# Kernel optimization log

Measured on AMD Instinct MI355X. Metric: run time of the kernel, lower is better.

## Reference

```python
import jax, jax.numpy as jnp
import numpy as np

IN_F, OUT_F = 128, 128
R, LEV, N = 2, 2, 8192
JD = (R - 1) * LEV + 1  # 3 filter levels


def setup_inputs() -> dict:
    key = jax.random.key(0)
    ks = jax.random.split(key, 7)
    x = jax.random.normal(ks[0], (N, IN_F), dtype=jnp.float32)
    d_list = jax.random.uniform(ks[1], (JD, N), dtype=jnp.float32)
    U = jax.random.normal(ks[2], (N, N), dtype=jnp.float32)
    Vt = jax.random.normal(ks[3], (N, N), dtype=jnp.float32)
    # learned params
    bound = float(np.sqrt(6.0 / (IN_F + OUT_F)))  # xavier_uniform
    weight = jax.random.uniform(ks[4], (IN_F, OUT_F), dtype=jnp.float32, minval=-bound, maxval=bound)
    filt = jax.random.uniform(ks[5], (JD, N), dtype=jnp.float32, minval=0.9, maxval=1.1)
    bias = jnp.zeros((OUT_F,), dtype=jnp.float32)
    return {"x": x, "d_list": d_list, "U": U, "Vt": Vt, "weight": weight, "filt": filt, "bias": bias}


def reference(x, d_list, U, Vt, weight, filt, bias):
    # Original loop: sum_j U @ ((d_j * f_j * d_j)[:, None] * (Vt @ (x @ W)))
    # By linearity this equals U @ ((sum_j d_j^2 * f_j)[:, None] * (Vt @ (x @ W)))
    # -- same math, with Vt@xw computed once and U applied once.
    xw = x @ weight                                  # [N, out]
    Vxw = Vt @ xw                                    # [N, out]
    scale = jnp.sum(d_list * filt * d_list, axis=0)  # [N]
    out = U @ (scale[:, None] * Vxw)                 # [N, out]
    return out + bias
```

## Files before the change

### kernel.cpp

```cpp
#include <hip/hip_runtime.h>

typedef short s8v __attribute__((ext_vector_type(8)));
typedef float f32x4 __attribute__((ext_vector_type(4)));

#define BM 32
#define KC 64
#define PAD 72

__device__ __forceinline__ unsigned short f2bf(float x) {
    unsigned int u = __float_as_uint(x);
    u += 0x7fffu + ((u >> 16) & 1u);
    return (unsigned short)(u >> 16);
}

__global__ __launch_bounds__(256, 2) void gemm_kernel(
    const float* __restrict__ A, int lda,
    const unsigned short* __restrict__ Bt, int ldb,
    float* __restrict__ C, int klen)
{
    __shared__ __align__(16) unsigned short As[2][BM * PAD];
    __shared__ __align__(16) unsigned short Bs[2][128 * PAD];

    const int t    = threadIdx.x;
    const int wave = t >> 6;
    const int lane = t & 63;
    const int quad = lane >> 4;
    const int l16  = lane & 15;

    const int mbase = blockIdx.x * BM;
    const int k0    = blockIdx.y * klen;
    C += (size_t)blockIdx.y * gridDim.x * BM * 128;

    const int ar  = t >> 3;
    const int akg = (t & 7) * 8;
    const float*          Ap = A  + (size_t)(mbase + ar) * lda + k0 + akg;
    const unsigned short* Bp = Bt + (size_t)ar * ldb + k0 + akg;

    const int nchunks = klen / KC;

    {
        float4 a0 = *(const float4*)(Ap);
        float4 a1 = *(const float4*)(Ap + 4);
        s8v b0 = *(const s8v*)(Bp);
        s8v b1 = *(const s8v*)(Bp + (size_t)32 * ldb);
        s8v b2 = *(const s8v*)(Bp + (size_t)64 * ldb);
        s8v b3 = *(const s8v*)(Bp + (size_t)96 * ldb);
        s8v av;
        av[0] = (short)f2bf(a0.x); av[1] = (short)f2bf(a0.y);
        av[2] = (short)f2bf(a0.z); av[3] = (short)f2bf(a0.w);
        av[4] = (short)f2bf(a1.x); av[5] = (short)f2bf(a1.y);
        av[6] = (short)f2bf(a1.z); av[7] = (short)f2bf(a1.w);
        *(s8v*)&As[0][ar * PAD + akg] = av;
        *(s8v*)&Bs[0][(ar +  0) * PAD + akg] = b0;
        *(s8v*)&Bs[0][(ar + 32) * PAD + akg] = b1;
        *(s8v*)&Bs[0][(ar + 64) * PAD + akg] = b2;
        *(s8v*)&Bs[0][(ar + 96) * PAD + akg] = b3;
    }
    __syncthreads();

    f32x4 acc00 = {0.f,0.f,0.f,0.f}, acc01 = {0.f,0.f,0.f,0.f};
    f32x4 acc10 = {0.f,0.f,0.f,0.f}, acc11 = {0.f,0.f,0.f,0.f};

    const int arow0 = l16 * PAD;
    const int arow1 = (16 + l16) * PAD;
    const int brow0 = (wave * 32 + l16) * PAD;
    const int brow1 = (wave * 32 + 16 + l16) * PAD;
    const int kq    = quad * 8;

    for (int c = 0; c < nchunks; ++c) {
        const int  cur = c & 1;
        const bool pf  = (c + 1 < nchunks);
        float4 a0, a1; s8v b0, b1, b2, b3;
        if (pf) {
            const size_t o = (size_t)(c + 1) * KC;
            a0 = *(const float4*)(Ap + o);
            a1 = *(const float4*)(Ap + o + 4);
            b0 = *(const s8v*)(Bp + o);
            b1 = *(const s8v*)(Bp + o + (size_t)32 * ldb);
            b2 = *(const s8v*)(Bp + o + (size_t)64 * ldb);
            b3 = *(const s8v*)(Bp + o + (size_t)96 * ldb);
        }
        const unsigned short* as = As[cur];
        const unsigned short* bs = Bs[cur];
        #pragma unroll
        for (int kk = 0; kk < 2; ++kk) {
            const int ko = kk * 32 + kq;
            s8v af0 = *(const s8v*)&as[arow0 + ko];
            s8v af1 = *(const s8v*)&as[arow1 + ko];
            s8v bg0 = *(const s8v*)&bs[brow0 + ko];
            s8v bg1 = *(const s8v*)&bs[brow1 + ko];
            acc00 = __builtin_amdgcn_mfma_f32_16x16x32_bf16(af0, bg0, acc00, 0, 0, 0);
            acc01 = __builtin_amdgcn_mfma_f32_16x16x32_bf16(af0, bg1, acc01, 0, 0, 0);
            acc10 = __builtin_amdgcn_mfma_f32_16x16x32_bf16(af1, bg0, acc10, 0, 0, 0);
            acc11 = __builtin_amdgcn_mfma_f32_16x16x32_bf16(af1, bg1, acc11, 0, 0, 0);
        }
        if (pf) {
            const int nb = cur ^ 1;
            s8v av;
            av[0] = (short)f2bf(a0.x); av[1] = (short)f2bf(a0.y);
            av[2] = (short)f2bf(a0.z); av[3] = (short)f2bf(a0.w);
            av[4] = (short)f2bf(a1.x); av[5] = (short)f2bf(a1.y);
            av[6] = (short)f2bf(a1.z); av[7] = (short)f2bf(a1.w);
            *(s8v*)&As[nb][ar * PAD + akg] = av;
            *(s8v*)&Bs[nb][(ar +  0) * PAD + akg] = b0;
            *(s8v*)&Bs[nb][(ar + 32) * PAD + akg] = b1;
            *(s8v*)&Bs[nb][(ar + 64) * PAD + akg] = b2;
            *(s8v*)&Bs[nb][(ar + 96) * PAD + akg] = b3;
        }
        __syncthreads();
    }

    const int col = wave * 32 + l16;
    const int row = mbase + quad * 4;
    #pragma unroll
    for (int i = 0; i < 4; ++i) {
        C[(size_t)(row + i)      * 128 + col]      = acc00[i];
        C[(size_t)(row + i)      * 128 + col + 16] = acc01[i];
        C[(size_t)(row + 16 + i) * 128 + col]      = acc10[i];
        C[(size_t)(row + 16 + i) * 128 + col + 16] = acc11[i];
    }
}

__global__ __launch_bounds__(256) void tkern(
    const float* __restrict__ a, const float* __restrict__ b,
    const float* __restrict__ dl, const float* __restrict__ ft,
    unsigned short* __restrict__ out, int nrows, int mode)
{
    __shared__ __align__(16) unsigned short L[128 * PAD];
    const int t    = threadIdx.x;
    const int kb   = blockIdx.x * 64;
    const int kloc = t >> 2;
    const int fseg = (t & 3) * 32;
    const int k    = kb + kloc;

    float s = 1.0f;
    if (mode) {
        float s0 = 0.f;
        #pragma unroll
        for (int j = 0; j < 3; ++j) {
            float d = dl[(size_t)j * nrows + k];
            s0 += d * d * ft[(size_t)j * nrows + k];
        }
        s = s0;
    }
    const float* ap = a + (size_t)k * 128 + fseg;
    const float* bp = b + (size_t)k * 128 + fseg;
    #pragma unroll
    for (int i = 0; i < 8; ++i) {
        float4 v = *(const float4*)(ap + i * 4);
        if (mode) {
            float4 w = *(const float4*)(bp + i * 4);
            v.x += w.x; v.y += w.y; v.z += w.z; v.w += w.w;
        }
        const int fb = fseg + i * 4;
        L[(fb + 0) * PAD + kloc] = f2bf(v.x * s);
        L[(fb + 1) * PAD + kloc] = f2bf(v.y * s);
        L[(fb + 2) * PAD + kloc] = f2bf(v.z * s);
        L[(fb + 3) * PAD + kloc] = f2bf(v.w * s);
    }
    __syncthreads();
    const int f    = t >> 1;
    const int half = (t & 1) * 32;
    unsigned short* op = out + (size_t)f * nrows + kb + half;
    #pragma unroll
    for (int i = 0; i < 4; ++i) {
        *(s8v*)(op + i * 8) = *(const s8v*)&L[f * PAD + half + i * 8];
    }
}

__global__ __launch_bounds__(256) void addbias_kernel(
    const float* __restrict__ p0, const float* __restrict__ p1,
    const float* __restrict__ bias, float* __restrict__ out)
{
    const size_t e = ((size_t)blockIdx.x * 256 + threadIdx.x) * 4;
    float4 x = *(const float4*)(p0 + e);
    float4 y = *(const float4*)(p1 + e);
    float4 bb = *(const float4*)(bias + (e & 127));
    float4 r;
    r.x = x.x + y.x + bb.x;
    r.y = x.y + y.y + bb.y;
    r.z = x.z + y.z + bb.z;
    r.w = x.w + y.w + bb.w;
    *(float4*)(out + e) = r;
}

extern "C" void kernel_launch(void* const* d_in, const int* in_sizes, int n_in,
                              void* d_out, int out_size, void* d_ws, size_t ws_size,
                              hipStream_t stream)
{
    const float* x  = (const float*)d_in[0];
    const float* dl = (const float*)d_in[1];
    const float* U  = (const float*)d_in[2];
    const float* Vt = (const float*)d_in[3];
    const float* W  = (const float*)d_in[4];
    const float* ft = (const float*)d_in[5];
    const float* bs = (const float*)d_in[6];
    float* out = (float*)d_out;

    const int N = 8192, F = 128;
    char* ws = (char*)d_ws;
    unsigned short* Wt  = (unsigned short*)(ws);
    unsigned short* xwt = (unsigned short*)(ws + (64 << 10));
    unsigned short* yt  = (unsigned short*)(ws + (64 << 10) + (2 << 20));
    float* bufA = (float*)(ws + (64 << 10) + (4 << 20));
    float* bufB = (float*)(ws + (64 << 10) + (12 << 20));

    tkern<<<dim3(F / 64), 256, 0, stream>>>(W, nullptr, nullptr, nullptr, Wt, F, 0);
    gemm_kernel<<<dim3(N / BM, 1), 256, 0, stream>>>(x, F, Wt, F, bufA, F);
    tkern<<<dim3(N / 64), 256, 0, stream>>>(bufA, nullptr, nullptr, nullptr, xwt, N, 0);
    gemm_kernel<<<dim3(N / BM, 2), 256, 0, stream>>>(Vt, N, xwt, N, bufB, N / 2);
    tkern<<<dim3(N / 64), 256, 0, stream>>>(bufB, bufB + (size_t)N * F, dl, ft, yt, N, 1);
    gemm_kernel<<<dim3(N / BM, 2), 256, 0, stream>>>(U, N, yt, N, bufA, N / 2);
    addbias_kernel<<<dim3((N * F) / (256 * 4)), 256, 0, stream>>>(
        bufA, bufA + (size_t)N * F, bs, out);
}
```

Baseline: 601.4 us.

## Replace LDS-tiled GEMM with register-streaming MFMA kernel and 4-way split-K

The shared-memory double-buffered GEMM is replaced by a kernel in which each wave loads its A rows (fp32, converted to bf16 in registers) and all 128 B columns straight from global memory into registers. Loads are ping-ponged across two register sets, and each wave computes a 32x128 tile with 16 accumulators. This removes LDS traffic and block-level barriers. Split-K rises from 2 to 4 slabs, and the transpose and final-reduce kernels now sum a variable number of slabs. The cost is much higher register pressure (occupancy 1), no B reuse across the four waves of a block (each wave reloads B from L2), and extra partial-sum memory traffic from the wider split.

```diff
diff --git a/kernel.cpp b/kernel.cpp
--- a/kernel.cpp
+++ b/kernel.cpp
@@ -3,8 +3,6 @@
 typedef short s8v __attribute__((ext_vector_type(8)));
 typedef float f32x4 __attribute__((ext_vector_type(4)));
 
-#define BM 32
-#define KC 64
 #define PAD 72
 
 __device__ __forceinline__ unsigned short f2bf(float x) {
@@ -13,118 +11,99 @@
     return (unsigned short)(u >> 16);
 }
 
-__global__ __launch_bounds__(256, 2) void gemm_kernel(
+
+struct ASet { float4 a[4]; };
+struct BSet { s8v  b[8];  };
+
+__device__ __forceinline__ void loadA(ASet& S, const float* Ap0, const float* Ap1, int ko) {
+    S.a[0] = *(const float4*)(Ap0 + ko);
+    S.a[1] = *(const float4*)(Ap0 + ko + 4);
+    S.a[2] = *(const float4*)(Ap1 + ko);
+    S.a[3] = *(const float4*)(Ap1 + ko + 4);
+}
+
+__device__ __forceinline__ void loadB(BSet& S, const unsigned short* Bp, int ko, int ldb) {
+    #pragma unroll
+    for (int nt = 0; nt < 8; ++nt)
+        S.b[nt] = *(const s8v*)(Bp + (size_t)nt * 16 * ldb + ko);
+}
+
+__device__ __forceinline__ s8v cvt8(float4 lo, float4 hi) {
+    s8v r;
+    r[0] = (short)f2bf(lo.x); r[1] = (short)f2bf(lo.y);
+    r[2] = (short)f2bf(lo.z); r[3] = (short)f2bf(lo.w);
+    r[4] = (short)f2bf(hi.x); r[5] = (short)f2bf(hi.y);
+    r[6] = (short)f2bf(hi.z); r[7] = (short)f2bf(hi.w);
+    return r;
+}
+
+__device__ __forceinline__ void compute(f32x4 (&acc)[2][8], const ASet& AS, const BSet& BS) {
+    s8v af0 = cvt8(AS.a[0], AS.a[1]);
+    s8v af1 = cvt8(AS.a[2], AS.a[3]);
+    #pragma unroll
+    for (int nt = 0; nt < 8; ++nt) {
+        acc[0][nt] = __builtin_amdgcn_mfma_f32_16x16x32_bf16(af0, BS.b[nt], acc[0][nt], 0, 0, 0);
+        acc[1][nt] = __builtin_amdgcn_mfma_f32_16x16x32_bf16(af1, BS.b[nt], acc[1][nt], 0, 0, 0);
+    }
+}
+
+__global__ __launch_bounds__(256, 1) void gemm_stream(
     const float* __restrict__ A, int lda,
     const unsigned short* __restrict__ Bt, int ldb,
     float* __restrict__ C, int klen)
 {
-    __shared__ __align__(16) unsigned short As[2][BM * PAD];
-    __shared__ __align__(16) unsigned short Bs[2][128 * PAD];
-
     const int t    = threadIdx.x;
     const int wave = t >> 6;
     const int lane = t & 63;
     const int quad = lane >> 4;
     const int l16  = lane & 15;
 
-    const int mbase = blockIdx.x * BM;
+    const int mbase = blockIdx.x * 128 + wave * 32;
     const int k0    = blockIdx.y * klen;
-    C += (size_t)blockIdx.y * gridDim.x * BM * 128;
+    C += (size_t)blockIdx.y * ((size_t)gridDim.x * 128 * 128);
 
-    const int ar  = t >> 3;
-    const int akg = (t & 7) * 8;
-    const float*          Ap = A  + (size_t)(mbase + ar) * lda + k0 + akg;
-    const unsigned short* Bp = Bt + (size_t)ar * ldb + k0 + akg;
+    const float* Ap0 = A + (size_t)(mbase + l16) * lda + k0 + quad * 8;
+    const float* Ap1 = Ap0 + (size_t)16 * lda;
+    const unsigned short* Bp = Bt + (size_t)l16 * ldb + k0 + quad * 8;
 
-    const int nchunks = klen / KC;
+    const int nsteps = klen / 32;
 
-    {
-        float4 a0 = *(const float4*)(Ap);
-        float4 a1 = *(const float4*)(Ap + 4);
-        s8v b0 = *(const s8v*)(Bp);
-        s8v b1 = *(const s8v*)(Bp + (size_t)32 * ldb);
-        s8v b2 = *(const s8v*)(Bp + (size_t)64 * ldb);
-        s8v b3 = *(const s8v*)(Bp + (size_t)96 * ldb);
-        s8v av;
-        av[0] = (short)f2bf(a0.x); av[1] = (short)f2bf(a0.y);
-        av[2] = (short)f2bf(a0.z); av[3] = (short)f2bf(a0.w);
-        av[4] = (short)f2bf(a1.x); av[5] = (short)f2bf(a1.y);
-        av[6] = (short)f2bf(a1.z); av[7] = (short)f2bf(a1.w);
-        *(s8v*)&As[0][ar * PAD + akg] = av;
-        *(s8v*)&Bs[0][(ar +  0) * PAD + akg] = b0;
-        *(s8v*)&Bs[0][(ar + 32) * PAD + akg] = b1;
-        *(s8v*)&Bs[0][(ar + 64) * PAD + akg] = b2;
-        *(s8v*)&Bs[0][(ar + 96) * PAD + akg] = b3;
+    f32x4 acc[2][8];
+    #pragma unroll
+    for (int m = 0; m < 2; ++m)
+        #pragma unroll
+        for (int n = 0; n < 8; ++n)
+            acc[m][n] = (f32x4){0.f, 0.f, 0.f, 0.f};
+
+    ASet Ae, Ao; BSet Be, Bo;
+    loadA(Ae, Ap0, Ap1, 0);   loadB(Be, Bp, 0, ldb);
+    loadA(Ao, Ap0, Ap1, 32);  loadB(Bo, Bp, 32, ldb);
+
+    for (int s = 0; s < nsteps - 2; s += 2) {
+        compute(acc, Ae, Be);
+        loadA(Ae, Ap0, Ap1, (s + 2) * 32);
+        loadB(Be, Bp, (s + 2) * 32, ldb);
+        compute(acc, Ao, Bo);
+        loadA(Ao, Ap0, Ap1, (s + 3) * 32);
+        loadB(Bo, Bp, (s + 3) * 32, ldb);
     }
-    __syncthreads();
+    compute(acc, Ae, Be);
+    compute(acc, Ao, Bo);
 
-    f32x4 acc00 = {0.f,0.f,0.f,0.f}, acc01 = {0.f,0.f,0.f,0.f};
-    f32x4 acc10 = {0.f,0.f,0.f,0.f}, acc11 = {0.f,0.f,0.f,0.f};
-
-    const int arow0 = l16 * PAD;
-    const int arow1 = (16 + l16) * PAD;
-    const int brow0 = (wave * 32 + l16) * PAD;
-    const int brow1 = (wave * 32 + 16 + l16) * PAD;
-    const int kq    = quad * 8;
-
-    for (int c = 0; c < nchunks; ++c) {
-        const int  cur = c & 1;
-        const bool pf  = (c + 1 < nchunks);
-        float4 a0, a1; s8v b0, b1, b2, b3;
-        if (pf) {
-            const size_t o = (size_t)(c + 1) * KC;
-            a0 = *(const float4*)(Ap + o);
-            a1 = *(const float4*)(Ap + o + 4);
-            b0 = *(const s8v*)(Bp + o);
-            b1 = *(const s8v*)(Bp + o + (size_t)32 * ldb);
-            b2 = *(const s8v*)(Bp + o + (size_t)64 * ldb);
-            b3 = *(const s8v*)(Bp + o + (size_t)96 * ldb);
-        }
-        const unsigned short* as = As[cur];
-        const unsigned short* bs = Bs[cur];
+    const int row0 = mbase + quad * 4;
+    #pragma unroll
+    for (int m = 0; m < 2; ++m)
         #pragma unroll
-        for (int kk = 0; kk < 2; ++kk) {
-            const int ko = kk * 32 + kq;
-            s8v af0 = *(const s8v*)&as[arow0 + ko];
-            s8v af1 = *(const s8v*)&as[arow1 + ko];
-            s8v bg0 = *(const s8v*)&bs[brow0 + ko];
-            s8v bg1 = *(const s8v*)&bs[brow1 + ko];
-            acc00 = __builtin_amdgcn_mfma_f32_16x16x32_bf16(af0, bg0, acc00, 0, 0, 0);
-            acc01 = __builtin_amdgcn_mfma_f32_16x16x32_bf16(af0, bg1, acc01, 0, 0, 0);
-            acc10 = __builtin_amdgcn_mfma_f32_16x16x32_bf16(af1, bg0, acc10, 0, 0, 0);
-            acc11 = __builtin_amdgcn_mfma_f32_16x16x32_bf16(af1, bg1, acc11, 0, 0, 0);
-        }
-        if (pf) {
-            const int nb = cur ^ 1;
-            s8v av;
-            av[0] = (short)f2bf(a0.x); av[1] = (short)f2bf(a0.y);
-            av[2] = (short)f2bf(a0.z); av[3] = (short)f2bf(a0.w);
-            av[4] = (short)f2bf(a1.x); av[5] = (short)f2bf(a1.y);
-            av[6] = (short)f2bf(a1.z); av[7] = (short)f2bf(a1.w);
-            *(s8v*)&As[nb][ar * PAD + akg] = av;
-            *(s8v*)&Bs[nb][(ar +  0) * PAD + akg] = b0;
-            *(s8v*)&Bs[nb][(ar + 32) * PAD + akg] = b1;
-            *(s8v*)&Bs[nb][(ar + 64) * PAD + akg] = b2;
-            *(s8v*)&Bs[nb][(ar + 96) * PAD + akg] = b3;
-        }
-        __syncthreads();
-    }
-
-    const int col = wave * 32 + l16;
-    const int row = mbase + quad * 4;
-    #pragma unroll
-    for (int i = 0; i < 4; ++i) {
-        C[(size_t)(row + i)      * 128 + col]      = acc00[i];
-        C[(size_t)(row + i)      * 128 + col + 16] = acc01[i];
-        C[(size_t)(row + 16 + i) * 128 + col]      = acc10[i];
-        C[(size_t)(row + 16 + i) * 128 + col + 16] = acc11[i];
-    }
+        for (int nt = 0; nt < 8; ++nt)
+            #pragma unroll
+            for (int i = 0; i < 4; ++i)
+                C[(size_t)(row0 + m * 16 + i) * 128 + nt * 16 + l16] = acc[m][nt][i];
 }
 
 __global__ __launch_bounds__(256) void tkern(
-    const float* __restrict__ a, const float* __restrict__ b,
+    const float* __restrict__ a,
     const float* __restrict__ dl, const float* __restrict__ ft,
-    unsigned short* __restrict__ out, int nrows, int mode)
+    unsigned short* __restrict__ out, int nrows, int nslab, int mode)
 {
     __shared__ __align__(16) unsigned short L[128 * PAD];
     const int t    = threadIdx.x;
@@ -143,13 +122,13 @@
         }
         s = s0;
     }
+    const size_t sstride = (size_t)nrows * 128;
     const float* ap = a + (size_t)k * 128 + fseg;
-    const float* bp = b + (size_t)k * 128 + fseg;
     #pragma unroll
     for (int i = 0; i < 8; ++i) {
         float4 v = *(const float4*)(ap + i * 4);
-        if (mode) {
-            float4 w = *(const float4*)(bp + i * 4);
+        for (int sl = 1; sl < nslab; ++sl) {
+            float4 w = *(const float4*)(ap + (size_t)sl * sstride + i * 4);
             v.x += w.x; v.y += w.y; v.z += w.z; v.w += w.w;
         }
         const int fb = fseg + i * 4;
@@ -163,24 +142,21 @@
     const int half = (t & 1) * 32;
     unsigned short* op = out + (size_t)f * nrows + kb + half;
     #pragma unroll
-    for (int i = 0; i < 4; ++i) {
+    for (int i = 0; i < 4; ++i)
         *(s8v*)(op + i * 8) = *(const s8v*)&L[f * PAD + half + i * 8];
-    }
 }
 
-__global__ __launch_bounds__(256) void addbias_kernel(
-    const float* __restrict__ p0, const float* __restrict__ p1,
-    const float* __restrict__ bias, float* __restrict__ out)
+__global__ __launch_bounds__(256) void reduce_bias(
+    const float* __restrict__ p, const float* __restrict__ bias,
+    float* __restrict__ out, int nslab)
 {
-    const size_t e = ((size_t)blockIdx.x * 256 + threadIdx.x) * 4;
-    float4 x = *(const float4*)(p0 + e);
-    float4 y = *(const float4*)(p1 + e);
-    float4 bb = *(const float4*)(bias + (e & 127));
-    float4 r;
-    r.x = x.x + y.x + bb.x;
-    r.y = x.y + y.y + bb.y;
-    r.z = x.z + y.z + bb.z;
-    r.w = x.w + y.w + bb.w;
+    const size_t NF = (size_t)8192 * 128;
+    const size_t e  = ((size_t)blockIdx.x * 256 + threadIdx.x) * 4;
+    float4 r = *(const float4*)(bias + (e & 127));
+    for (int s = 0; s < nslab; ++s) {
+        float4 x = *(const float4*)(p + (size_t)s * NF + e);
+        r.x += x.x; r.y += x.y; r.z += x.z; r.w += x.w;
+    }
     *(float4*)(out + e) = r;
 }
 
@@ -202,15 +178,13 @@
     unsigned short* Wt  = (unsigned short*)(ws);
     unsigned short* xwt = (unsigned short*)(ws + (64 << 10));
     unsigned short* yt  = (unsigned short*)(ws + (64 << 10) + (2 << 20));
-    float* bufA = (float*)(ws + (64 << 10) + (4 << 20));
-    float* bufB = (float*)(ws + (64 << 10) + (12 << 20));
+    float* P = (float*)(ws + (64 << 10) + (4 << 20));
 
-    tkern<<<dim3(F / 64), 256, 0, stream>>>(W, nullptr, nullptr, nullptr, Wt, F, 0);
-    gemm_kernel<<<dim3(N / BM, 1), 256, 0, stream>>>(x, F, Wt, F, bufA, F);
-    tkern<<<dim3(N / 64), 256, 0, stream>>>(bufA, nullptr, nullptr, nullptr, xwt, N, 0);
-    gemm_kernel<<<dim3(N / BM, 2), 256, 0, stream>>>(Vt, N, xwt, N, bufB, N / 2);
-    tkern<<<dim3(N / 64), 256, 0, stream>>>(bufB, bufB + (size_t)N * F, dl, ft, yt, N, 1);
-    gemm_kernel<<<dim3(N / BM, 2), 256, 0, stream>>>(U, N, yt, N, bufA, N / 2);
-    addbias_kernel<<<dim3((N * F) / (256 * 4)), 256, 0, stream>>>(
-        bufA, bufA + (size_t)N * F, bs, out);
+    tkern<<<dim3(F / 64), 256, 0, stream>>>(W, nullptr, nullptr, Wt, F, 1, 0);
+    gemm_stream<<<dim3(N / 128, 1), 256, 0, stream>>>(x, F, Wt, F, P, F);
+    tkern<<<dim3(N / 64), 256, 0, stream>>>(P, nullptr, nullptr, xwt, N, 1, 0);
+    gemm_stream<<<dim3(N / 128, 4), 256, 0, stream>>>(Vt, N, xwt, N, P, N / 4);
+    tkern<<<dim3(N / 64), 256, 0, stream>>>(P, dl, ft, yt, N, 4, 1);
+    gemm_stream<<<dim3(N / 128, 4), 256, 0, stream>>>(U, N, yt, N, P, N / 4);
+    reduce_bias<<<dim3((N * F) / (256 * 4)), 256, 0, stream>>>(P, bs, out, 4);
 }
```

Result: slower. 628.9 us (+4.6%).
